# Performance work log

Measured on AMD Instinct MI355X. Metric: run time of the kernel, lower is better.

Reference implementation:

```python
import jax, jax.numpy as jnp
import numpy as np

B, S, HID, NH, HD = 2, 2048, 1024, 16, 64
SCALE = 1.0 / np.sqrt(HD)
NEG = -1e9


def _rope_cache(seq_len, dim, base=10000.0):
    inv_freq = 1.0 / (base ** (np.arange(0, dim, 2, dtype=np.float32) / dim))
    t = np.arange(seq_len, dtype=np.float32)
    freqs = np.outer(t, inv_freq)                      # [S, dim/2]
    emb = np.concatenate([freqs, freqs], axis=-1)      # [S, dim]
    return jnp.asarray(np.cos(emb)), jnp.asarray(np.sin(emb))


def _rotate_half(x):
    x1, x2 = jnp.split(x, 2, axis=-1)
    return jnp.concatenate([-x2, x1], axis=-1)


def setup_inputs() -> dict:
    key = jax.random.key(0)
    k0, k1, k2, k3, k4 = jax.random.split(key, 5)
    hidden_states = jax.random.normal(k0, (B, S, HID), jnp.float32)
    Wq = jax.random.normal(k1, (HID, NH * HD), jnp.float32) * 0.02
    Wk = jax.random.normal(k2, (HID, NH * HD), jnp.float32) * 0.02
    Wv = jax.random.normal(k3, (HID, NH * HD), jnp.float32) * 0.02
    Wo = jax.random.normal(k4, (NH * HD, HID), jnp.float32) * 0.02
    causal = jnp.tril(jnp.ones((S, S), bool))
    attention_mask = jnp.broadcast_to(
        jnp.where(causal, 0.0, NEG).astype(jnp.float32)[None, None], (B, 1, S, S))
    position_ids = jnp.broadcast_to(jnp.arange(S, dtype=jnp.int32)[None], (B, S))
    cos, sin = _rope_cache(S, HD)
    return {"hidden_states": hidden_states, "attention_mask": attention_mask,
            "position_ids": position_ids, "cos": cos, "sin": sin,
            "Wq": Wq, "Wk": Wk, "Wv": Wv, "Wo": Wo}


def reference(hidden_states, attention_mask, position_ids, cos, sin, Wq, Wk, Wv, Wo):
    b, s, _ = hidden_states.shape
    def proj(W):  # [B,S,HID] @ [HID,NH*HD] -> [B,NH,S,HD]
        return jnp.einsum('bsh,hd->bsd', hidden_states, W).reshape(b, s, NH, HD).transpose(0, 2, 1, 3)
    q, k, v = proj(Wq), proj(Wk), proj(Wv)
    # RoPE: gather per-position cos/sin -> [B,1,S,HD]
    cos_g = cos[position_ids][:, None]
    sin_g = sin[position_ids][:, None]
    q = q * cos_g + _rotate_half(q) * sin_g
    k = k * cos_g + _rotate_half(k) * sin_g
    scores = jnp.einsum('bhqd,bhkd->bhqk', q, k) * SCALE + attention_mask
    attn = jax.nn.softmax(scores.astype(jnp.float32), axis=-1).astype(q.dtype)
    out = jnp.einsum('bhqk,bhkd->bhqd', attn, v)
    out = out.transpose(0, 2, 1, 3).reshape(b, s, NH * HD)
    return jnp.einsum('bsd,dh->bsh', out, Wo)
```

## Files before the change

kernel.cpp:

```cpp
#include <hip/hip_runtime.h>

typedef __bf16 bf16x8 __attribute__((ext_vector_type(8)));
typedef float  f32x4  __attribute__((ext_vector_type(4)));
typedef unsigned short ushortx8 __attribute__((ext_vector_type(8)));
typedef unsigned short ushortx4 __attribute__((ext_vector_type(4)));

static __device__ __forceinline__ unsigned short f2bf(float f) {
  unsigned int u = __builtin_bit_cast(unsigned int, f);
  u += 0x7FFFu + ((u >> 16) & 1u);
  return (unsigned short)(u >> 16);
}
static __device__ __forceinline__ unsigned short f2bf_fast(float f) {
  unsigned int u = __builtin_bit_cast(unsigned int, f);
  return (unsigned short)((u + 0x8000u) >> 16);
}

#define GLL16(gp, lp) __builtin_amdgcn_global_load_lds(                       \
    (const __attribute__((address_space(1))) void*)(gp),                      \
    (__attribute__((address_space(3))) void*)(lp), 16, 0, 0)

__global__ __launch_bounds__(256) void prep_kernel(const float* __restrict__ X,
                                                   const float* __restrict__ W0,
                                                   const float* __restrict__ W1,
                                                   const float* __restrict__ W2,
                                                   const float* __restrict__ W3,
                                                   unsigned short* __restrict__ Xbf,
                                                   unsigned short* __restrict__ D0,
                                                   unsigned short* __restrict__ D1,
                                                   unsigned short* __restrict__ D2,
                                                   unsigned short* __restrict__ D3) {
  int z = blockIdx.z;
  if (z >= 4) {
    long bid = (long)(z - 4) * 1024 + blockIdx.y * 32 + blockIdx.x;
    int tl = threadIdx.y * 32 + threadIdx.x;
    long i = bid * 2048 + (long)tl * 8;
    float4 f0 = *(const float4*)(X + i);
    float4 f1 = *(const float4*)(X + i + 4);
    ushortx8 u;
    u[0] = f2bf(f0.x); u[1] = f2bf(f0.y); u[2] = f2bf(f0.z); u[3] = f2bf(f0.w);
    u[4] = f2bf(f1.x); u[5] = f2bf(f1.y); u[6] = f2bf(f1.z); u[7] = f2bf(f1.w);
    *(ushortx8*)(Xbf + i) = u;
    return;
  }
  const float* src = (z == 0) ? W0 : (z == 1) ? W1 : (z == 2) ? W2 : W3;
  unsigned short* dst = (z == 0) ? D0 : (z == 1) ? D1 : (z == 2) ? D2 : D3;
  const int R = 1024, C = 1024;
  __shared__ unsigned short t[32][33];
  int c = blockIdx.x * 32 + threadIdx.x;
#pragma unroll
  for (int i = 0; i < 4; ++i) {
    int r = blockIdx.y * 32 + threadIdx.y + i * 8;
    t[threadIdx.y + i * 8][threadIdx.x] = f2bf(src[(size_t)r * C + c]);
  }
  __syncthreads();
  int rr = blockIdx.y * 32 + threadIdx.x;
#pragma unroll
  for (int i = 0; i < 4; ++i) {
    int cc = blockIdx.x * 32 + threadIdx.y + i * 8;
    dst[(size_t)cc * R + rr] = t[threadIdx.x][threadIdx.y + i * 8];
  }
}

__global__ __launch_bounds__(256) void gemm128_kernel(
    const unsigned short* __restrict__ A,
    const unsigned short* __restrict__ BT0,
    const unsigned short* __restrict__ BT1,
    const unsigned short* __restrict__ BT2,
    unsigned short* __restrict__ outQ,
    unsigned short* __restrict__ outK,
    unsigned short* __restrict__ outVT,
    const int* __restrict__ pos_ids,
    const float* __restrict__ cosb,
    const float* __restrict__ sinb) {
  const int K = 1024;
  int id = blockIdx.x + 8 * (blockIdx.y + 32 * blockIdx.z);
  int m_idx = id & 31;
  int nzi = id >> 5;
  int n_idx = nzi & 7;
  int z = nzi >> 3;
  const unsigned short* BT = (z == 0) ? BT0 : (z == 1 ? BT1 : BT2);
  int n0 = n_idx * 128, m0 = m_idx * 128;
  int t = threadIdx.x, lane = t & 63, w = t >> 6;
  int wy = w >> 1, wx = w & 1;
  int n16 = lane & 15, quad = lane >> 4;
  __shared__ __align__(16) unsigned short sA0[128 * 32];
  __shared__ __align__(16) unsigned short sA1[128 * 32];
  __shared__ __align__(16) unsigned short sB0[128 * 32];
  __shared__ __align__(16) unsigned short sB1[128 * 32];

  int r4 = lane >> 2, c4 = lane & 3;
  const char* gA = (const char*)(A + (size_t)(m0 + w * 32 + r4) * K) + ((c4 ^ (r4 & 3)) * 16);
  const char* gB = (const char*)(BT + (size_t)(n0 + w * 32 + r4) * K) + ((c4 ^ (r4 & 3)) * 16);
  const size_t row16 = (size_t)16 * K * 2;

  f32x4 acc[4][4];
#pragma unroll
  for (int i = 0; i < 4; ++i)
#pragma unroll
    for (int j = 0; j < 4; ++j) acc[i][j] = f32x4{0.f, 0.f, 0.f, 0.f};

#define GSTAGE(kk_, SA, SB)                                                     \
  do {                                                                          \
    GLL16(gA + (size_t)(kk_) * 2, SA + (w * 32) * 32);                          \
    GLL16(gA + (size_t)(kk_) * 2 + row16, SA + (w * 32 + 16) * 32);             \
    GLL16(gB + (size_t)(kk_) * 2, SB + (w * 32) * 32);                          \
    GLL16(gB + (size_t)(kk_) * 2 + row16, SB + (w * 32 + 16) * 32);             \
  } while (0)

#define GCOMPUTE(SA, SB)                                                        \
  do {                                                                          \
    bf16x8 a[4], b[4];                                                          \
    int cs = (quad ^ (n16 & 3)) * 8;                                            \
    _Pragma("unroll") for (int i = 0; i < 4; ++i) {                             \
      a[i] = *(const bf16x8*)(&SA[(wy * 64 + i * 16 + n16) * 32 + cs]);         \
      b[i] = *(const bf16x8*)(&SB[(wx * 64 + i * 16 + n16) * 32 + cs]);         \
    }                                                                           \
    _Pragma("unroll") for (int mt = 0; mt < 4; ++mt)                            \
      _Pragma("unroll") for (int nt = 0; nt < 4; ++nt)                          \
        acc[mt][nt] = __builtin_amdgcn_mfma_f32_16x16x32_bf16(                  \
            a[mt], b[nt], acc[mt][nt], 0, 0, 0);                                \
  } while (0)

  GSTAGE(0, sA0, sB0);
  for (int kk = 0; kk < K;) {
    __syncthreads();
    if (kk + 32 < K) GSTAGE(kk + 32, sA1, sB1);
    GCOMPUTE(sA0, sB0);
    kk += 32;
    if (kk >= K) break;
    __syncthreads();
    if (kk + 32 < K) GSTAGE(kk + 32, sA0, sB0);
    GCOMPUTE(sA1, sB1);
    kk += 32;
  }
#undef GSTAGE
#undef GCOMPUTE

  if (z < 2) {
    const float qs = (z == 0) ? (0.125f * 1.44269504088896340736f) : 1.0f;
#pragma unroll
    for (int mt = 0; mt < 4; ++mt)
#pragma unroll
      for (int r = 0; r < 4; ++r) {
        int row = m0 + wy * 64 + mt * 16 + quad * 4 + r;
        int b = row >> 11, s = row & 2047;
        int pos = pos_ids[b * 2048 + s];
        const float* cb = cosb + (size_t)pos * 64;
        const float* sb = sinb + (size_t)pos * 64;
#pragma unroll
        for (int nt = 0; nt < 2; ++nt) {
          int d0 = nt * 16 + n16;
          float c0 = cb[d0] * qs, s0 = sb[d0] * qs;
          float c1 = cb[d0 + 32] * qs, s1 = sb[d0 + 32] * qs;
          float x0 = acc[mt][nt][r], x1 = acc[mt][nt + 2][r];
          acc[mt][nt][r]     = x0 * c0 - x1 * s0;
          acc[mt][nt + 2][r] = x1 * c1 + x0 * s1;
        }
      }
  }

  if (z == 2) {
#pragma unroll
    for (int mt = 0; mt < 4; ++mt)
#pragma unroll
      for (int nt = 0; nt < 4; ++nt) {
        int row = m0 + wy * 64 + mt * 16 + quad * 4;
        int b = row >> 11, s = row & 2047;
        int col = n0 + wx * 64 + nt * 16 + n16;
        int h = col >> 6, d = col & 63;
        ushortx4 u;
#pragma unroll
        for (int r = 0; r < 4; ++r) u[r] = f2bf(acc[mt][nt][r]);
        *(ushortx4*)(&outVT[(((size_t)b * 16 + h) * 64 + d) * 2048 + s]) = u;
      }
    return;
  }

#pragma unroll
  for (int mt = 0; mt < 4; ++mt)
#pragma unroll
    for (int nt = 0; nt < 4; ++nt)
#pragma unroll
      for (int r = 0; r < 4; ++r) {
        int row = m0 + wy * 64 + mt * 16 + quad * 4 + r;
        int col = n0 + wx * 64 + nt * 16 + n16;
        unsigned short* dst = (z == 0) ? outQ : outK;
        int b = row >> 11, s = row & 2047, h = col >> 6, d = col & 63;
        dst[(((size_t)b * 16 + h) * 2048 + s) * 64 + d] = f2bf(acc[mt][nt][r]);
      }
}

__global__ __launch_bounds__(256) void gemm64_kernel(const unsigned short* __restrict__ A,
                                                     const unsigned short* __restrict__ BT,
                                                     float* __restrict__ outF) {
  const int K = 1024, N = 1024;
  int m0 = blockIdx.x * 64, n0 = blockIdx.y * 64;
  int t = threadIdx.x, lane = t & 63, w = t >> 6;
  int wy = w >> 1, wx = w & 1;
  int n16 = lane & 15, quad = lane >> 4;
  __shared__ __align__(16) unsigned short sA0[64 * 32];
  __shared__ __align__(16) unsigned short sA1[64 * 32];
  __shared__ __align__(16) unsigned short sB0[64 * 32];
  __shared__ __align__(16) unsigned short sB1[64 * 32];

  int r4 = lane >> 2, c4 = lane & 3;
  const char* gA = (const char*)(A + (size_t)(m0 + w * 16 + r4) * K) + ((c4 ^ (r4 & 3)) * 16);
  const char* gB = (const char*)(BT + (size_t)(n0 + w * 16 + r4) * K) + ((c4 ^ (r4 & 3)) * 16);

  f32x4 acc[2][2];
#pragma unroll
  for (int i = 0; i < 2; ++i)
#pragma unroll
    for (int j = 0; j < 2; ++j) acc[i][j] = f32x4{0.f, 0.f, 0.f, 0.f};

#define WSTAGE(kk_, SA, SB)                                                     \
  do {                                                                          \
    GLL16(gA + (size_t)(kk_) * 2, SA + (w * 16) * 32);                          \
    GLL16(gB + (size_t)(kk_) * 2, SB + (w * 16) * 32);                          \
  } while (0)

#define WCOMPUTE(SA, SB)                                                        \
  do {                                                                          \
    int cs = (quad ^ (n16 & 3)) * 8;                                            \
    bf16x8 a0 = *(const bf16x8*)(&SA[(wy * 32 + n16) * 32 + cs]);               \
    bf16x8 a1 = *(const bf16x8*)(&SA[(wy * 32 + 16 + n16) * 32 + cs]);          \
    bf16x8 b0 = *(const bf16x8*)(&SB[(wx * 32 + n16) * 32 + cs]);               \
    bf16x8 b1 = *(const bf16x8*)(&SB[(wx * 32 + 16 + n16) * 32 + cs]);          \
    acc[0][0] = __builtin_amdgcn_mfma_f32_16x16x32_bf16(a0, b0, acc[0][0], 0, 0, 0); \
    acc[0][1] = __builtin_amdgcn_mfma_f32_16x16x32_bf16(a0, b1, acc[0][1], 0, 0, 0); \
    acc[1][0] = __builtin_amdgcn_mfma_f32_16x16x32_bf16(a1, b0, acc[1][0], 0, 0, 0); \
    acc[1][1] = __builtin_amdgcn_mfma_f32_16x16x32_bf16(a1, b1, acc[1][1], 0, 0, 0); \
  } while (0)

  WSTAGE(0, sA0, sB0);
  for (int kk = 0; kk < K;) {
    __syncthreads();
    if (kk + 32 < K) WSTAGE(kk + 32, sA1, sB1);
    WCOMPUTE(sA0, sB0);
    kk += 32;
    if (kk >= K) break;
    __syncthreads();
    if (kk + 32 < K) WSTAGE(kk + 32, sA0, sB0);
    WCOMPUTE(sA1, sB1);
    kk += 32;
  }
#undef WSTAGE
#undef WCOMPUTE

#pragma unroll
  for (int mt = 0; mt < 2; ++mt)
#pragma unroll
    for (int nt = 0; nt < 2; ++nt)
#pragma unroll
      for (int r = 0; r < 4; ++r) {
        int row = m0 + wy * 32 + mt * 16 + quad * 4 + r;
        int col = n0 + wx * 32 + nt * 16 + n16;
        outF[(size_t)row * N + col] = acc[mt][nt][r];
      }
}

__global__ __launch_bounds__(512) void attn_kernel(const unsigned short* __restrict__ Q,
                                                   const unsigned short* __restrict__ Kk,
                                                   const unsigned short* __restrict__ VT,
                                                   unsigned short* __restrict__ O) {
  int bh = blockIdx.x;
  int qt = (int)(gridDim.y - 1 - blockIdx.y);
  int t = threadIdx.x;
  int lane = t & 63;
  int w = t >> 6;
  int g = w >> 2;
  int w4 = w & 3;
  int n16 = lane & 15, quad = lane >> 4;
  int r8 = lane >> 3, c8 = lane & 7;
  const unsigned short* Qb = Q + (size_t)bh * 2048 * 64;
  const unsigned short* Kb = Kk + (size_t)bh * 2048 * 64;
  const unsigned short* Vb = VT + (size_t)bh * 64 * 2048;

  __shared__ __align__(16) unsigned short sKV[2 * 2 * 2 * 4096];
  __shared__ __align__(16) unsigned short sP[8][16 * 64];
  unsigned short* spW = sP[w];
  unsigned short* gBase = sKV + g * 16384;

  int b_ = bh >> 4, h_ = bh & 15;
  int nk = qt + 1;
  int u = (nk + 1) >> 1;
  int beg = g ? u : 0;
  int end = g ? nk : u;
  int qg = qt * 64 + w4 * 16 + n16;

  bf16x8 aQ[2];
#pragma unroll
  for (int kb = 0; kb < 2; ++kb)
    aQ[kb] = *(const bf16x8*)(Qb + (size_t)qg * 64 + kb * 32 + quad * 8);

  f32x4 o[4];
  float mst = -3e38f, lst = 0.f;
#pragma unroll
  for (int ct = 0; ct < 4; ++ct) o[ct] = f32x4{0.f, 0.f, 0.f, 0.f};

#define ASTAGE(kt_, BUF)                                                                  \
  do {                                                                                    \
    const unsigned short* kg_ = Kb + (size_t)((kt_) * 64 + w4 * 16) * 64;                 \
    const unsigned short* vg_ = Vb + (size_t)(w4 * 16) * 2048 + (kt_) * 64;               \
    unsigned short* dK = gBase + (BUF) * 8192 + (w4 * 16) * 64;                           \
    unsigned short* dV = dK + 4096;                                                       \
    GLL16(kg_ + (size_t)r8 * 64 + (c8 ^ r8) * 8, dK);                                     \
    GLL16(kg_ + (size_t)(8 + r8) * 64 + (c8 ^ r8) * 8, dK + 8 * 64);                      \
    GLL16(vg_ + (size_t)r8 * 2048 + (c8 ^ r8) * 8, dV);                                   \
    GLL16(vg_ + (size_t)(8 + r8) * 2048 + (c8 ^ r8) * 8, dV + 8 * 64);                    \
  } while (0)

#define ACOMPUTE(kt_, BUF)                                                                \
  do {                                                                                    \
    const unsigned short* kT_ = gBase + (BUF) * 8192;                                     \
    const unsigned short* vT_ = kT_ + 4096;                                               \
    f32x4 sc[4];                                \
    _Pragma("unroll") for (int mt = 0; mt < 4; ++mt) {                                    \
      const unsigned short* kr = &kT_[(mt * 16 + n16) * 64];                              \
      bf16x8 ka0 = *(const bf16x8*)(kr + ((quad ^ (n16 & 7)) * 8));                       \
      bf16x8 ka1 = *(const bf16x8*)(kr + (((4 + quad) ^ (n16 & 7)) * 8));                 \
      f32x4 zv = f32x4{0.f, 0.f, 0.f, 0.f};                                               \
      zv = __builtin_amdgcn_mfma_f32_16x16x32_bf16(ka0, aQ[0], zv, 0, 0, 0);              \
      sc[mt] = __builtin_amdgcn_mfma_f32_16x16x32_bf16(ka1, aQ[1], zv, 0, 0, 0);          \
    }                                                                                     \
    float p[4][4];                                                                        \
    _Pragma("unroll") for (int mt = 0; mt < 4; ++mt)                                      \
      _Pragma("unroll") for (int r = 0; r < 4; ++r) p[mt][r] = sc[mt][r];                 \
    if ((kt_) == nk - 1) {                                 \
      int kb0 = (kt_) * 64 + quad * 4;                                                    \
      _Pragma("unroll") for (int mt = 0; mt < 4; ++mt)                                    \
        _Pragma("unroll") for (int r = 0; r < 4; ++r)                                     \
          if (kb0 + mt * 16 + r > qg) p[mt][r] = -3e38f;                                  \
    }                                                                                     \
    float rm = p[0][0];                                                                   \
    _Pragma("unroll") for (int mt = 0; mt < 4; ++mt)                                      \
      _Pragma("unroll") for (int r = 0; r < 4; ++r) rm = fmaxf(rm, p[mt][r]);             \
    rm = fmaxf(rm, __shfl_xor(rm, 16));                                                   \
    rm = fmaxf(rm, __shfl_xor(rm, 32));                                                   \
    float mn = fmaxf(mst, rm);                                                            \
    float al = exp2f(mst - mn);                                                           \
    mst = mn;                                                                             \
    float rs = 0.f;                                                                       \
    _Pragma("unroll") for (int mt = 0; mt < 4; ++mt)                                      \
      _Pragma("unroll") for (int r = 0; r < 4; ++r) {                                     \
        p[mt][r] = exp2f(p[mt][r] - mn);                                                  \
        rs += p[mt][r];                                                                   \
      }                                                                                   \
    lst = lst * al + rs;                                                                  \
    _Pragma("unroll") for (int ct = 0; ct < 4; ++ct)                                      \
      _Pragma("unroll") for (int r = 0; r < 4; ++r) o[ct][r] *= al;                       \
    _Pragma("unroll") for (int mt = 0; mt < 4; ++mt) {                                    \
      ushortx4 uu;                                                                        \
      _Pragma("unroll") for (int r = 0; r < 4; ++r) uu[r] = f2bf_fast(p[mt][r]);          \
      int ch = (mt * 2 + (quad >> 1)) ^ (n16 & 7);                                        \
      *(ushortx4*)(&spW[n16 * 64 + ch * 8 + (quad & 1) * 4]) = uu;                        \
    }                                                                                     \
    __builtin_amdgcn_s_waitcnt(0xC07F);     \
    bf16x8 aP0 = *(const bf16x8*)(&spW[n16 * 64 + ((quad ^ (n16 & 7)) * 8)]);             \
    bf16x8 aP1 = *(const bf16x8*)(&spW[n16 * 64 + (((4 + quad) ^ (n16 & 7)) * 8)]);       \
    _Pragma("unroll") for (int ct = 0; ct < 4; ++ct) {                                    \
      const unsigned short* vr = &vT_[(ct * 16 + n16) * 64];                              \
      bf16x8 va0 = *(const bf16x8*)(vr + ((quad ^ (n16 & 7)) * 8));                       \
      bf16x8 va1 = *(const bf16x8*)(vr + (((4 + quad) ^ (n16 & 7)) * 8));                 \
      o[ct] = __builtin_amdgcn_mfma_f32_16x16x32_bf16(va0, aP0, o[ct], 0, 0, 0);          \
      o[ct] = __builtin_amdgcn_mfma_f32_16x16x32_bf16(va1, aP1, o[ct], 0, 0, 0);          \
    }                                                                                     \
  } while (0)

  if (beg < end) ASTAGE(beg, 0);
  int it = 0;
  while (it < u) {
    __syncthreads();
    {
      int kt = beg + it;
      if (kt + 1 < end) ASTAGE(kt + 1, 1);
      if (kt < end) ACOMPUTE(kt, 0);
    }
    if (++it >= u) break;
    __syncthreads();
    {
      int kt = beg + it;
      if (kt + 1 < end) ASTAGE(kt + 1, 0);
      if (kt < end) ACOMPUTE(kt, 1);
    }
    ++it;
  }
#undef ASTAGE
#undef ACOMPUTE

  lst += __shfl_xor(lst, 16);
  lst += __shfl_xor(lst, 32);

  __syncthreads();
  float* scratch = (float*)sKV;
  int sidx = (w4 * 64 + lane) * 18;
  if (g == 1) {
#pragma unroll
    for (int ct = 0; ct < 4; ++ct)
#pragma unroll
      for (int r = 0; r < 4; ++r) scratch[sidx + ct * 4 + r] = o[ct][r];
    scratch[sidx + 16] = mst;
    scratch[sidx + 17] = lst;
  }
  __syncthreads();
  if (g == 0) {
    float m1 = scratch[sidx + 16], l1 = scratch[sidx + 17];
    float m = fmaxf(mst, m1);
    float a0 = exp2f(mst - m), a1 = exp2f(m1 - m);
    float inv = 1.0f / (lst * a0 + l1 * a1);
#pragma unroll
    for (int ct = 0; ct < 4; ++ct) {
      ushortx4 uo;
#pragma unroll
      for (int r = 0; r < 4; ++r) {
        float v = (o[ct][r] * a0 + scratch[sidx + ct * 4 + r] * a1) * inv;
        uo[r] = f2bf(v);
      }
      size_t addr = ((size_t)b_ * 2048 + qg) * 1024 + h_ * 64 + ct * 16 + quad * 4;
      *(ushortx4*)(&O[addr]) = uo;
    }
  }
}

extern "C" void kernel_launch(void* const* d_in, const int* in_sizes, int n_in,
                              void* d_out, int out_size, void* d_ws, size_t ws_size,
                              hipStream_t stream) {
  const float* X    = (const float*)d_in[0];
  const int*   pos  = (const int*)d_in[2];
  const float* cosb = (const float*)d_in[3];
  const float* sinb = (const float*)d_in[4];
  const float* Wq   = (const float*)d_in[5];
  const float* Wk   = (const float*)d_in[6];
  const float* Wv   = (const float*)d_in[7];
  const float* Wo   = (const float*)d_in[8];
  float* out = (float*)d_out;

  char* ws = (char*)d_ws;
  const size_t SZ_X = 4096UL * 1024 * 2;
  const size_t SZ_W = 1024UL * 1024 * 2;
  unsigned short* Xbf = (unsigned short*)(ws);
  unsigned short* WTq = (unsigned short*)(ws + SZ_X);
  unsigned short* WTk = (unsigned short*)(ws + SZ_X + SZ_W);
  unsigned short* WTv = (unsigned short*)(ws + SZ_X + 2 * SZ_W);
  unsigned short* WTo = (unsigned short*)(ws + SZ_X + 3 * SZ_W);
  unsigned short* Qbf = (unsigned short*)(ws + SZ_X + 4 * SZ_W);
  unsigned short* Kbf = (unsigned short*)(ws + 2 * SZ_X + 4 * SZ_W);
  unsigned short* VTr = (unsigned short*)(ws + 3 * SZ_X + 4 * SZ_W);
  unsigned short* Obf = (unsigned short*)(ws + 4 * SZ_X + 4 * SZ_W);

  prep_kernel<<<dim3(32, 32, 6), dim3(32, 8), 0, stream>>>(
      X, Wq, Wk, Wv, Wo, Xbf, WTq, WTk, WTv, WTo);

  gemm128_kernel<<<dim3(8, 32, 3), 256, 0, stream>>>(Xbf, WTq, WTk, WTv,
                                                     Qbf, Kbf, VTr,
                                                     pos, cosb, sinb);

  attn_kernel<<<dim3(32, 32), 512, 0, stream>>>(Qbf, Kbf, VTr, Obf);

  gemm64_kernel<<<dim3(64, 16), 256, 0, stream>>>(Obf, WTo, out);
}
```

Before: 209.9 us.

## Fuse all stages into one persistent cooperative kernel with grid syncs

Replaces the four separate launches (prep, QKV GEMM, attention, output GEMM) with a single cooperative kernel of 256 persistent blocks that separates the phases with grid.sync. The GEMMs now use a 3-buffer LDS ring with explicit vmcnt waits, and each block loops over the three projections. Attention blocks process several query tiles each, and the softmax skips the rescale when the running max grows by no more than a threshold. This targets launch gaps and tail effects, but each grid barrier costs time, the grid is limited to 256 blocks (fewer than the old grids), and the lazy rescale slightly changes numerics.

Result: slower. 480.2 us (+128.7%).

```diff
diff --git a/kernel.cpp b/kernel.cpp
--- a/kernel.cpp
+++ b/kernel.cpp
@@ -1,4 +1,7 @@
 #include <hip/hip_runtime.h>
+#include <hip/hip_cooperative_groups.h>
+
+namespace cg = cooperative_groups;
 
 typedef __bf16 bf16x8 __attribute__((ext_vector_type(8)));
 typedef float  f32x4  __attribute__((ext_vector_type(4)));
@@ -19,284 +22,218 @@
     (const __attribute__((address_space(1))) void*)(gp),                      \
     (__attribute__((address_space(3))) void*)(lp), 16, 0, 0)
 
-__global__ __launch_bounds__(256) void prep_kernel(const float* __restrict__ X,
-                                                   const float* __restrict__ W0,
-                                                   const float* __restrict__ W1,
-                                                   const float* __restrict__ W2,
-                                                   const float* __restrict__ W3,
-                                                   unsigned short* __restrict__ Xbf,
-                                                   unsigned short* __restrict__ D0,
-                                                   unsigned short* __restrict__ D1,
-                                                   unsigned short* __restrict__ D2,
-                                                   unsigned short* __restrict__ D3) {
-  int z = blockIdx.z;
-  if (z >= 4) {
-    long bid = (long)(z - 4) * 1024 + blockIdx.y * 32 + blockIdx.x;
-    int tl = threadIdx.y * 32 + threadIdx.x;
-    long i = bid * 2048 + (long)tl * 8;
-    float4 f0 = *(const float4*)(X + i);
-    float4 f1 = *(const float4*)(X + i + 4);
-    ushortx8 u;
-    u[0] = f2bf(f0.x); u[1] = f2bf(f0.y); u[2] = f2bf(f0.z); u[3] = f2bf(f0.w);
-    u[4] = f2bf(f1.x); u[5] = f2bf(f1.y); u[6] = f2bf(f1.z); u[7] = f2bf(f1.w);
-    *(ushortx8*)(Xbf + i) = u;
-    return;
-  }
-  const float* src = (z == 0) ? W0 : (z == 1) ? W1 : (z == 2) ? W2 : W3;
-  unsigned short* dst = (z == 0) ? D0 : (z == 1) ? D1 : (z == 2) ? D2 : D3;
-  const int R = 1024, C = 1024;
-  __shared__ unsigned short t[32][33];
-  int c = blockIdx.x * 32 + threadIdx.x;
-#pragma unroll
-  for (int i = 0; i < 4; ++i) {
-    int r = blockIdx.y * 32 + threadIdx.y + i * 8;
-    t[threadIdx.y + i * 8][threadIdx.x] = f2bf(src[(size_t)r * C + c]);
-  }
-  __syncthreads();
-  int rr = blockIdx.y * 32 + threadIdx.x;
-#pragma unroll
-  for (int i = 0; i < 4; ++i) {
-    int cc = blockIdx.x * 32 + threadIdx.y + i * 8;
-    dst[(size_t)cc * R + rr] = t[threadIdx.x][threadIdx.y + i * 8];
-  }
-}
-
-__global__ __launch_bounds__(256) void gemm128_kernel(
-    const unsigned short* __restrict__ A,
-    const unsigned short* __restrict__ BT0,
-    const unsigned short* __restrict__ BT1,
-    const unsigned short* __restrict__ BT2,
-    unsigned short* __restrict__ outQ,
-    unsigned short* __restrict__ outK,
-    unsigned short* __restrict__ outVT,
-    const int* __restrict__ pos_ids,
-    const float* __restrict__ cosb,
-    const float* __restrict__ sinb) {
+struct FusedParams {
+  const float* X;
+  const int* pos;
+  const float* cosb;
+  const float* sinb;
+  const float* Wq;
+  const float* Wk;
+  const float* Wv;
+  const float* Wo;
+  unsigned short* Xbf;
+  unsigned short* WTq;
+  unsigned short* WTk;
+  unsigned short* WTv;
+  unsigned short* WTo;
+  unsigned short* Qbf;
+  unsigned short* Kbf;
+  unsigned short* VTr;
+  unsigned short* Obf;
+  float* out;
+};
+
+__device__ __forceinline__ void gemm_ring128(
+    const unsigned short* __restrict__ A, const unsigned short* __restrict__ BT,
+    int m0, int n0, int t, f32x4 (&acc)[2][4],
+    unsigned short* sA, unsigned short* sB, unsigned short* sDm) {
   const int K = 1024;
-  int id = blockIdx.x + 8 * (blockIdx.y + 32 * blockIdx.z);
-  int m_idx = id & 31;
-  int nzi = id >> 5;
-  int n_idx = nzi & 7;
-  int z = nzi >> 3;
-  const unsigned short* BT = (z == 0) ? BT0 : (z == 1 ? BT1 : BT2);
-  int n0 = n_idx * 128, m0 = m_idx * 128;
-  int t = threadIdx.x, lane = t & 63, w = t >> 6;
+  const int BUFE = 128 * 32;
+  int lane = t & 63, w = t >> 6;
   int wy = w >> 1, wx = w & 1;
   int n16 = lane & 15, quad = lane >> 4;
-  __shared__ __align__(16) unsigned short sA0[128 * 32];
-  __shared__ __align__(16) unsigned short sA1[128 * 32];
-  __shared__ __align__(16) unsigned short sB0[128 * 32];
-  __shared__ __align__(16) unsigned short sB1[128 * 32];
-
-  int r4 = lane >> 2, c4 = lane & 3;
-  const char* gA = (const char*)(A + (size_t)(m0 + w * 32 + r4) * K) + ((c4 ^ (r4 & 3)) * 16);
-  const char* gB = (const char*)(BT + (size_t)(n0 + w * 32 + r4) * K) + ((c4 ^ (r4 & 3)) * 16);
-  const size_t row16 = (size_t)16 * K * 2;
-
-  f32x4 acc[4][4];
-#pragma unroll
-  for (int i = 0; i < 4; ++i)
-#pragma unroll
-    for (int j = 0; j < 4; ++j) acc[i][j] = f32x4{0.f, 0.f, 0.f, 0.f};
-
-#define GSTAGE(kk_, SA, SB)                                                     \
+  int schunk = (lane & 3) ^ ((lane >> 2) & 3);
+  const unsigned short* gA0 = A + (size_t)(m0 + w * 16 + (lane >> 2)) * K + schunk * 8;
+  const unsigned short* gB0 = BT + (size_t)(n0 + w * 16 + (lane >> 2)) * K + schunk * 8;
+  unsigned short* stA = sA + (w * 16) * 32;
+  unsigned short* stB = sB + (w * 16) * 32;
+  int cs = (quad ^ (n16 & 3)) * 8;
+  const unsigned short* rdA = sA + (wy * 32 + n16) * 32 + cs;
+  const unsigned short* rdB = sB + (wx * 64 + n16) * 32 + cs;
+  bf16x8 a[2], bb[4];
+
+#define GSTG(tt, DA, DB)                                                        \
   do {                                                                          \
-    GLL16(gA + (size_t)(kk_) * 2, SA + (w * 32) * 32);                          \
-    GLL16(gA + (size_t)(kk_) * 2 + row16, SA + (w * 32 + 16) * 32);             \
-    GLL16(gB + (size_t)(kk_) * 2, SB + (w * 32) * 32);                          \
-    GLL16(gB + (size_t)(kk_) * 2 + row16, SB + (w * 32 + 16) * 32);             \
+    GLL16(gA0 + (size_t)(tt) * 32, (DA));                                       \
+    GLL16(gB0 + (size_t)(tt) * 32, (DB));                                       \
   } while (0)
-
-#define GCOMPUTE(SA, SB)                                                        \
+#define GRD(bufi)                                                               \
   do {                                                                          \
-    bf16x8 a[4], b[4];                                                          \
-    int cs = (quad ^ (n16 & 3)) * 8;                                            \
-    _Pragma("unroll") for (int i = 0; i < 4; ++i) {                             \
-      a[i] = *(const bf16x8*)(&SA[(wy * 64 + i * 16 + n16) * 32 + cs]);         \
-      b[i] = *(const bf16x8*)(&SB[(wx * 64 + i * 16 + n16) * 32 + cs]);         \
-    }                                                                           \
-    _Pragma("unroll") for (int mt = 0; mt < 4; ++mt)                            \
-      _Pragma("unroll") for (int nt = 0; nt < 4; ++nt)                          \
-        acc[mt][nt] = __builtin_amdgcn_mfma_f32_16x16x32_bf16(                  \
-            a[mt], b[nt], acc[mt][nt], 0, 0, 0);                                \
+    _Pragma("unroll") for (int i = 0; i < 2; ++i)                               \
+      a[i] = *(const bf16x8*)(rdA + (bufi) * BUFE + i * 16 * 32);               \
+    _Pragma("unroll") for (int j = 0; j < 4; ++j)                               \
+      bb[j] = *(const bf16x8*)(rdB + (bufi) * BUFE + j * 16 * 32);              \
   } while (0)
-
-  GSTAGE(0, sA0, sB0);
-  for (int kk = 0; kk < K;) {
-    __syncthreads();
-    if (kk + 32 < K) GSTAGE(kk + 32, sA1, sB1);
-    GCOMPUTE(sA0, sB0);
-    kk += 32;
-    if (kk >= K) break;
-    __syncthreads();
-    if (kk + 32 < K) GSTAGE(kk + 32, sA0, sB0);
-    GCOMPUTE(sA1, sB1);
-    kk += 32;
+#define GMM                                                                     \
+  do {                                                                          \
+    _Pragma("unroll") for (int i = 0; i < 2; ++i)                               \
+      _Pragma("unroll") for (int j = 0; j < 4; ++j)                             \
+        acc[i][j] = __builtin_amdgcn_mfma_f32_16x16x32_bf16(                    \
+            a[i], bb[j], acc[i][j], 0, 0, 0);                                   \
+  } while (0)
+
+  GSTG(0, stA, stB);
+  GSTG(1, stA + BUFE, stB + BUFE);
+  asm volatile("s_waitcnt vmcnt(2)" ::: "memory");
+  __builtin_amdgcn_s_barrier();
+
+#pragma unroll 3
+  for (int kt = 0; kt < 30; ++kt) {
+    int buf = kt % 3, pfb = (kt + 2) % 3;
+    GRD(buf);
+    GSTG(kt + 2, stA + pfb * BUFE, stB + pfb * BUFE);
+    GMM;
+    asm volatile("s_waitcnt vmcnt(2)" ::: "memory");
+    __builtin_amdgcn_s_barrier();
   }
-#undef GSTAGE
-#undef GCOMPUTE
-
-  if (z < 2) {
-    const float qs = (z == 0) ? (0.125f * 1.44269504088896340736f) : 1.0f;
-#pragma unroll
-    for (int mt = 0; mt < 4; ++mt)
-#pragma unroll
-      for (int r = 0; r < 4; ++r) {
-        int row = m0 + wy * 64 + mt * 16 + quad * 4 + r;
-        int b = row >> 11, s = row & 2047;
-        int pos = pos_ids[b * 2048 + s];
-        const float* cb = cosb + (size_t)pos * 64;
-        const float* sb = sinb + (size_t)pos * 64;
-#pragma unroll
-        for (int nt = 0; nt < 2; ++nt) {
-          int d0 = nt * 16 + n16;
-          float c0 = cb[d0] * qs, s0 = sb[d0] * qs;
-          float c1 = cb[d0 + 32] * qs, s1 = sb[d0 + 32] * qs;
-          float x0 = acc[mt][nt][r], x1 = acc[mt][nt + 2][r];
-          acc[mt][nt][r]     = x0 * c0 - x1 * s0;
-          acc[mt][nt + 2][r] = x1 * c1 + x0 * s1;
-        }
+  GRD(0);
+  GSTG(31, sDm, sDm);
+  GMM;
+  asm volatile("s_waitcnt vmcnt(2)" ::: "memory");
+  __builtin_amdgcn_s_barrier();
+  GRD(1);
+  GSTG(31, sDm, sDm);
+  GMM;
+  asm volatile("s_waitcnt vmcnt(0)" ::: "memory");
+#undef GSTG
+#undef GRD
+#undef GMM
+}
+
+__global__ __launch_bounds__(512, 2) void fused_kernel(FusedParams p) {
+  __shared__ __align__(16) unsigned char smem[81920];
+  cg::grid_group grid = cg::this_grid();
+  int b = blockIdx.x, t = threadIdx.x;
+  int lane = t & 63, w = t >> 6;
+  int n16 = lane & 15, quad = lane >> 4;
+
+  {
+    size_t base = ((size_t)b * 512 + t) * 8;
+#pragma unroll
+    for (int p4 = 0; p4 < 4; ++p4) {
+      size_t i = base + (size_t)p4 * (131072 * 8);
+      float4 f0 = *(const float4*)(p.X + i);
+      float4 f1 = *(const float4*)(p.X + i + 4);
+      ushortx8 u;
+      u[0] = f2bf(f0.x); u[1] = f2bf(f0.y); u[2] = f2bf(f0.z); u[3] = f2bf(f0.w);
+      u[4] = f2bf(f1.x); u[5] = f2bf(f1.y); u[6] = f2bf(f1.z); u[7] = f2bf(f1.w);
+      *(ushortx8*)(p.Xbf + i) = u;
+    }
+    unsigned short (*tl)[32][33] = (unsigned short (*)[32][33])smem;
+    int sub = t >> 8;
+    int t256 = t & 255;
+    int tx = t256 & 31, ty = t256 >> 5;
+    for (int it = 0; it < 8; ++it) {
+      int tid = b * 16 + it * 2 + sub;
+      int mat = tid >> 10, rem = tid & 1023;
+      int trow = rem >> 5, tcol = rem & 31;
+      const float* src = (mat == 0) ? p.Wq : (mat == 1) ? p.Wk : (mat == 2) ? p.Wv : p.Wo;
+      unsigned short* dst = (mat == 0) ? p.WTq : (mat == 1) ? p.WTk : (mat == 2) ? p.WTv : p.WTo;
+#pragma unroll
+      for (int r = 0; r < 4; ++r)
+        tl[sub][ty + r * 8][tx] = f2bf(src[(size_t)(trow * 32 + ty + r * 8) * 1024 + tcol * 32 + tx]);
+      __syncthreads();
+#pragma unroll
+      for (int r = 0; r < 4; ++r)
+        dst[(size_t)(tcol * 32 + ty + r * 8) * 1024 + trow * 32 + tx] = tl[sub][tx][ty + r * 8];
+      __syncthreads();
+    }
+  }
+  __threadfence();
+  grid.sync();
+
+  {
+    unsigned short* sA = (unsigned short*)smem;
+    unsigned short* sB = (unsigned short*)(smem + 24576);
+    unsigned short* sDm = (unsigned short*)(smem + 49152);
+    int m0 = (b & 31) * 128, n0 = ((b >> 5) & 7) * 128;
+    int wy = w >> 1, wx = w & 1;
+    for (int z = 0; z < 3; ++z) {
+      if (z) __syncthreads();
+      const unsigned short* BTz = (z == 0) ? p.WTq : (z == 1 ? p.WTk : p.WTv);
+      f32x4 acc[2][4];
+#pragma unroll
+      for (int i = 0; i < 2; ++i)
+#pragma unroll
+        for (int j = 0; j < 4; ++j) acc[i][j] = f32x4{0.f, 0.f, 0.f, 0.f};
+      gemm_ring128(p.Xbf, BTz, m0, n0, t, acc, sA, sB, sDm);
+
+      if (z < 2) {
+        const float qs = (z == 0) ? (0.125f * 1.44269504088896340736f) : 1.0f;
+#pragma unroll
+        for (int mt = 0; mt < 2; ++mt)
+#pragma unroll
+          for (int r = 0; r < 4; ++r) {
+            int row = m0 + wy * 32 + mt * 16 + quad * 4 + r;
+            int b_ = row >> 11, s_ = row & 2047;
+            int pos = p.pos[b_ * 2048 + s_];
+            const float* cb = p.cosb + (size_t)pos * 64;
+            const float* sb = p.sinb + (size_t)pos * 64;
+#pragma unroll
+            for (int nt = 0; nt < 2; ++nt) {
+              int d0 = nt * 16 + n16;
+              float c0 = cb[d0] * qs, s0 = sb[d0] * qs;
+              float c1 = cb[d0 + 32] * qs, s1 = sb[d0 + 32] * qs;
+              float x0 = acc[mt][nt][r], x1 = acc[mt][nt + 2][r];
+              acc[mt][nt][r]     = x0 * c0 - x1 * s0;
+              acc[mt][nt + 2][r] = x1 * c1 + x0 * s1;
+            }
+          }
+        unsigned short* dst = (z == 0) ? p.Qbf : p.Kbf;
+#pragma unroll
+        for (int mt = 0; mt < 2; ++mt)
+#pragma unroll
+          for (int nt = 0; nt < 4; ++nt)
+#pragma unroll
+            for (int r = 0; r < 4; ++r) {
+              int row = m0 + wy * 32 + mt * 16 + quad * 4 + r;
+              int col = n0 + wx * 64 + nt * 16 + n16;
+              int b_ = row >> 11, s_ = row & 2047, h_ = col >> 6, d_ = col & 63;
+              dst[(((size_t)b_ * 16 + h_) * 2048 + s_) * 64 + d_] = f2bf(acc[mt][nt][r]);
+            }
+      } else {
+#pragma unroll
+        for (int mt = 0; mt < 2; ++mt)
+#pragma unroll
+          for (int nt = 0; nt < 4; ++nt) {
+            int row = m0 + wy * 32 + mt * 16 + quad * 4;
+            int b_ = row >> 11, s_ = row & 2047;
+            int col = n0 + wx * 64 + nt * 16 + n16;
+            int h_ = col >> 6, d_ = col & 63;
+            ushortx4 u;
+#pragma unroll
+            for (int r = 0; r < 4; ++r) u[r] = f2bf(acc[mt][nt][r]);
+            *(ushortx4*)(&p.VTr[(((size_t)b_ * 16 + h_) * 64 + d_) * 2048 + s_]) = u;
+          }
       }
+    }
   }
-
-  if (z == 2) {
-#pragma unroll
-    for (int mt = 0; mt < 4; ++mt)
-#pragma unroll
-      for (int nt = 0; nt < 4; ++nt) {
-        int row = m0 + wy * 64 + mt * 16 + quad * 4;
-        int b = row >> 11, s = row & 2047;
-        int col = n0 + wx * 64 + nt * 16 + n16;
-        int h = col >> 6, d = col & 63;
-        ushortx4 u;
-#pragma unroll
-        for (int r = 0; r < 4; ++r) u[r] = f2bf(acc[mt][nt][r]);
-        *(ushortx4*)(&outVT[(((size_t)b * 16 + h) * 64 + d) * 2048 + s]) = u;
-      }
-    return;
-  }
-
-#pragma unroll
-  for (int mt = 0; mt < 4; ++mt)
-#pragma unroll
-    for (int nt = 0; nt < 4; ++nt)
-#pragma unroll
-      for (int r = 0; r < 4; ++r) {
-        int row = m0 + wy * 64 + mt * 16 + quad * 4 + r;
-        int col = n0 + wx * 64 + nt * 16 + n16;
-        unsigned short* dst = (z == 0) ? outQ : outK;
-        int b = row >> 11, s = row & 2047, h = col >> 6, d = col & 63;
-        dst[(((size_t)b * 16 + h) * 2048 + s) * 64 + d] = f2bf(acc[mt][nt][r]);
-      }
-}
-
-__global__ __launch_bounds__(256) void gemm64_kernel(const unsigned short* __restrict__ A,
-                                                     const unsigned short* __restrict__ BT,
-                                                     float* __restrict__ outF) {
-  const int K = 1024, N = 1024;
-  int m0 = blockIdx.x * 64, n0 = blockIdx.y * 64;
-  int t = threadIdx.x, lane = t & 63, w = t >> 6;
-  int wy = w >> 1, wx = w & 1;
-  int n16 = lane & 15, quad = lane >> 4;
-  __shared__ __align__(16) unsigned short sA0[64 * 32];
-  __shared__ __align__(16) unsigned short sA1[64 * 32];
-  __shared__ __align__(16) unsigned short sB0[64 * 32];
-  __shared__ __align__(16) unsigned short sB1[64 * 32];
-
-  int r4 = lane >> 2, c4 = lane & 3;
-  const char* gA = (const char*)(A + (size_t)(m0 + w * 16 + r4) * K) + ((c4 ^ (r4 & 3)) * 16);
-  const char* gB = (const char*)(BT + (size_t)(n0 + w * 16 + r4) * K) + ((c4 ^ (r4 & 3)) * 16);
-
-  f32x4 acc[2][2];
-#pragma unroll
-  for (int i = 0; i < 2; ++i)
-#pragma unroll
-    for (int j = 0; j < 2; ++j) acc[i][j] = f32x4{0.f, 0.f, 0.f, 0.f};
-
-#define WSTAGE(kk_, SA, SB)                                                     \
-  do {                                                                          \
-    GLL16(gA + (size_t)(kk_) * 2, SA + (w * 16) * 32);                          \
-    GLL16(gB + (size_t)(kk_) * 2, SB + (w * 16) * 32);                          \
-  } while (0)
-
-#define WCOMPUTE(SA, SB)                                                        \
-  do {                                                                          \
-    int cs = (quad ^ (n16 & 3)) * 8;                                            \
-    bf16x8 a0 = *(const bf16x8*)(&SA[(wy * 32 + n16) * 32 + cs]);               \
-    bf16x8 a1 = *(const bf16x8*)(&SA[(wy * 32 + 16 + n16) * 32 + cs]);          \
-    bf16x8 b0 = *(const bf16x8*)(&SB[(wx * 32 + n16) * 32 + cs]);               \
-    bf16x8 b1 = *(const bf16x8*)(&SB[(wx * 32 + 16 + n16) * 32 + cs]);          \
-    acc[0][0] = __builtin_amdgcn_mfma_f32_16x16x32_bf16(a0, b0, acc[0][0], 0, 0, 0); \
-    acc[0][1] = __builtin_amdgcn_mfma_f32_16x16x32_bf16(a0, b1, acc[0][1], 0, 0, 0); \
-    acc[1][0] = __builtin_amdgcn_mfma_f32_16x16x32_bf16(a1, b0, acc[1][0], 0, 0, 0); \
-    acc[1][1] = __builtin_amdgcn_mfma_f32_16x16x32_bf16(a1, b1, acc[1][1], 0, 0, 0); \
-  } while (0)
-
-  WSTAGE(0, sA0, sB0);
-  for (int kk = 0; kk < K;) {
-    __syncthreads();
-    if (kk + 32 < K) WSTAGE(kk + 32, sA1, sB1);
-    WCOMPUTE(sA0, sB0);
-    kk += 32;
-    if (kk >= K) break;
-    __syncthreads();
-    if (kk + 32 < K) WSTAGE(kk + 32, sA0, sB0);
-    WCOMPUTE(sA1, sB1);
-    kk += 32;
-  }
-#undef WSTAGE
-#undef WCOMPUTE
-
-#pragma unroll
-  for (int mt = 0; mt < 2; ++mt)
-#pragma unroll
-    for (int nt = 0; nt < 2; ++nt)
-#pragma unroll
-      for (int r = 0; r < 4; ++r) {
-        int row = m0 + wy * 32 + mt * 16 + quad * 4 + r;
-        int col = n0 + wx * 32 + nt * 16 + n16;
-        outF[(size_t)row * N + col] = acc[mt][nt][r];
-      }
-}
-
-__global__ __launch_bounds__(512) void attn_kernel(const unsigned short* __restrict__ Q,
-                                                   const unsigned short* __restrict__ Kk,
-                                                   const unsigned short* __restrict__ VT,
-                                                   unsigned short* __restrict__ O) {
-  int bh = blockIdx.x;
-  int qt = (int)(gridDim.y - 1 - blockIdx.y);
-  int t = threadIdx.x;
-  int lane = t & 63;
-  int w = t >> 6;
-  int g = w >> 2;
-  int w4 = w & 3;
-  int n16 = lane & 15, quad = lane >> 4;
-  int r8 = lane >> 3, c8 = lane & 7;
-  const unsigned short* Qb = Q + (size_t)bh * 2048 * 64;
-  const unsigned short* Kb = Kk + (size_t)bh * 2048 * 64;
-  const unsigned short* Vb = VT + (size_t)bh * 64 * 2048;
-
-  __shared__ __align__(16) unsigned short sKV[2 * 2 * 2 * 4096];
-  __shared__ __align__(16) unsigned short sP[8][16 * 64];
-  unsigned short* spW = sP[w];
-  unsigned short* gBase = sKV + g * 16384;
-
-  int b_ = bh >> 4, h_ = bh & 15;
-  int nk = qt + 1;
-  int u = (nk + 1) >> 1;
-  int beg = g ? u : 0;
-  int end = g ? nk : u;
-  int qg = qt * 64 + w4 * 16 + n16;
-
-  bf16x8 aQ[2];
-#pragma unroll
-  for (int kb = 0; kb < 2; ++kb)
-    aQ[kb] = *(const bf16x8*)(Qb + (size_t)qg * 64 + kb * 32 + quad * 8);
-
-  f32x4 o[4];
-  float mst = -3e38f, lst = 0.f;
-#pragma unroll
-  for (int ct = 0; ct < 4; ++ct) o[ct] = f32x4{0.f, 0.f, 0.f, 0.f};
+  __threadfence();
+  grid.sync();
+
+  {
+    unsigned short* sKV = (unsigned short*)smem;
+    unsigned short* sP = (unsigned short*)(smem + 65536);
+    int g = w >> 2, w4 = w & 3;
+    int r8 = lane >> 3, c8 = lane & 7;
+    unsigned short* spW = sP + w * 1024;
+    unsigned short* gBase = sKV + g * 16384;
+    int slot = b & 7, bh = b >> 3;
+    int b_ = bh >> 4, h_ = bh & 15;
+    const unsigned short* Qb = p.Qbf + (size_t)bh * 2048 * 64;
+    const unsigned short* Kb = p.Kbf + (size_t)bh * 2048 * 64;
+    const unsigned short* Vb = p.VTr + (size_t)bh * 64 * 2048;
+    int qts[4] = {31 - slot, 16 + slot, 15 - slot, slot};
 
 #define ASTAGE(kt_, BUF)                                                                  \
   do {                                                                                    \
@@ -323,35 +260,38 @@
       zv = __builtin_amdgcn_mfma_f32_16x16x32_bf16(ka0, aQ[0], zv, 0, 0, 0);              \
       sc[mt] = __builtin_amdgcn_mfma_f32_16x16x32_bf16(ka1, aQ[1], zv, 0, 0, 0);          \
     }                                                                                     \
-    float p[4][4];                                                                        \
+    float pp[4][4];                                                                       \
     _Pragma("unroll") for (int mt = 0; mt < 4; ++mt)                                      \
-      _Pragma("unroll") for (int r = 0; r < 4; ++r) p[mt][r] = sc[mt][r];                 \
+      _Pragma("unroll") for (int r = 0; r < 4; ++r) pp[mt][r] = sc[mt][r];                \
     if ((kt_) == nk - 1) {                                 \
       int kb0 = (kt_) * 64 + quad * 4;                                                    \
       _Pragma("unroll") for (int mt = 0; mt < 4; ++mt)                                    \
         _Pragma("unroll") for (int r = 0; r < 4; ++r)                                     \
-          if (kb0 + mt * 16 + r > qg) p[mt][r] = -3e38f;                                  \
+          if (kb0 + mt * 16 + r > qg) pp[mt][r] = -3e38f;                                 \
     }                                                                                     \
-    float rm = p[0][0];                                                                   \
+    float rm = pp[0][0];                                                                  \
     _Pragma("unroll") for (int mt = 0; mt < 4; ++mt)                                      \
-      _Pragma("unroll") for (int r = 0; r < 4; ++r) rm = fmaxf(rm, p[mt][r]);             \
+      _Pragma("unroll") for (int r = 0; r < 4; ++r) rm = fmaxf(rm, pp[mt][r]);            \
     rm = fmaxf(rm, __shfl_xor(rm, 16));                                                   \
     rm = fmaxf(rm, __shfl_xor(rm, 32));                                                   \
-    float mn = fmaxf(mst, rm);                                                            \
-    float al = exp2f(mst - mn);                                                           \
-    mst = mn;                                                                             \
+    if (!__all(rm <= mst + 8.f)) {                                     \
+      float mn = fmaxf(mst, rm);                                                          \
+      float al = exp2f(mst - mn);                                                         \
+      mst = mn;                                                                           \
+      lst *= al;                                                                          \
+      _Pragma("unroll") for (int ct = 0; ct < 4; ++ct)                                    \
+        _Pragma("unroll") for (int r = 0; r < 4; ++r) o[ct][r] *= al;                     \
+    }                                                                                     \
     float rs = 0.f;                                                                       \
     _Pragma("unroll") for (int mt = 0; mt < 4; ++mt)                                      \
       _Pragma("unroll") for (int r = 0; r < 4; ++r) {                                     \
-        p[mt][r] = exp2f(p[mt][r] - mn);                                                  \
-        rs += p[mt][r];                                                                   \
+        pp[mt][r] = exp2f(pp[mt][r] - mst);                                               \
+        rs += pp[mt][r];                                                                  \
       }                                                                                   \
-    lst = lst * al + rs;                                                                  \
-    _Pragma("unroll") for (int ct = 0; ct < 4; ++ct)                                      \
-      _Pragma("unroll") for (int r = 0; r < 4; ++r) o[ct][r] *= al;                       \
+    lst += rs;                                                                            \
     _Pragma("unroll") for (int mt = 0; mt < 4; ++mt) {                                    \
       ushortx4 uu;                                                                        \
-      _Pragma("unroll") for (int r = 0; r < 4; ++r) uu[r] = f2bf_fast(p[mt][r]);          \
+      _Pragma("unroll") for (int r = 0; r < 4; ++r) uu[r] = f2bf_fast(pp[mt][r]);         \
       int ch = (mt * 2 + (quad >> 1)) ^ (n16 & 7);                                        \
       *(ushortx4*)(&spW[n16 * 64 + ch * 8 + (quad & 1) * 4]) = uu;                        \
     }                                                                                     \
@@ -367,58 +307,105 @@
     }                                                                                     \
   } while (0)
 
-  if (beg < end) ASTAGE(beg, 0);
-  int it = 0;
-  while (it < u) {
-    __syncthreads();
-    {
-      int kt = beg + it;
-      if (kt + 1 < end) ASTAGE(kt + 1, 1);
-      if (kt < end) ACOMPUTE(kt, 0);
+    for (int ui = 0; ui < 4; ++ui) {
+      __syncthreads();
+      int qt = qts[ui];
+      int nk = qt + 1;
+      int u = (nk + 1) >> 1;
+      int beg = g ? u : 0;
+      int end = g ? nk : u;
+      int qg = qt * 64 + w4 * 16 + n16;
+
+      bf16x8 aQ[2];
+#pragma unroll
+      for (int kb = 0; kb < 2; ++kb)
+        aQ[kb] = *(const bf16x8*)(Qb + (size_t)qg * 64 + kb * 32 + quad * 8);
+
+      f32x4 o[4];
+      float mst = -3e38f, lst = 0.f;
+#pragma unroll
+      for (int ct = 0; ct < 4; ++ct) o[ct] = f32x4{0.f, 0.f, 0.f, 0.f};
+
+      if (beg < end) ASTAGE(beg, 0);
+      int it = 0;
+      while (it < u) {
+        __syncthreads();
+        {
+          int kt = beg + it;
+          if (kt + 1 < end) ASTAGE(kt + 1, 1);
+          if (kt < end) ACOMPUTE(kt, 0);
+        }
+        if (++it >= u) break;
+        __syncthreads();
+        {
+          int kt = beg + it;
+          if (kt + 1 < end) ASTAGE(kt + 1, 0);
+          if (kt < end) ACOMPUTE(kt, 1);
+        }
+        ++it;
+      }
+
+      lst += __shfl_xor(lst, 16);
+      lst += __shfl_xor(lst, 32);
+
+      __syncthreads();
+      float* scratch = (float*)sKV;
+      int sidx = (w4 * 64 + lane) * 18;
+      if (g == 1) {
+#pragma unroll
+        for (int ct = 0; ct < 4; ++ct)
+#pragma unroll
+          for (int r = 0; r < 4; ++r) scratch[sidx + ct * 4 + r] = o[ct][r];
+        scratch[sidx + 16] = mst;
+        scratch[sidx + 17] = lst;
+      }
+      __syncthreads();
+      if (g == 0) {
+        float m1 = scratch[sidx + 16], l1 = scratch[sidx + 17];
+        float m = fmaxf(mst, m1);
+        float a0 = exp2f(mst - m), a1 = exp2f(m1 - m);
+        float inv = 1.0f / (lst * a0 + l1 * a1);
+#pragma unroll
+        for (int ct = 0; ct < 4; ++ct) {
+          ushortx4 uo;
+#pragma unroll
+          for (int r = 0; r < 4; ++r) {
+            float v = (o[ct][r] * a0 + scratch[sidx + ct * 4 + r] * a1) * inv;
+            uo[r] = f2bf(v);
+          }
+          size_t addr = ((size_t)b_ * 2048 + qg) * 1024 + h_ * 64 + ct * 16 + quad * 4;
+          *(ushortx4*)(&p.Obf[addr]) = uo;
+        }
+      }
     }
-    if (++it >= u) break;
-    __syncthreads();
-    {
-      int kt = beg + it;
-      if (kt + 1 < end) ASTAGE(kt + 1, 0);
-      if (kt < end) ACOMPUTE(kt, 1);
-    }
-    ++it;
-  }
 #undef ASTAGE
 #undef ACOMPUTE
-
-  lst += __shfl_xor(lst, 16);
-  lst += __shfl_xor(lst, 32);
-
-  __syncthreads();
-  float* scratch = (float*)sKV;
-  int sidx = (w4 * 64 + lane) * 18;
-  if (g == 1) {
-#pragma unroll
-    for (int ct = 0; ct < 4; ++ct)
-#pragma unroll
-      for (int r = 0; r < 4; ++r) scratch[sidx + ct * 4 + r] = o[ct][r];
-    scratch[sidx + 16] = mst;
-    scratch[sidx + 17] = lst;
   }
-  __syncthreads();
-  if (g == 0) {
-    float m1 = scratch[sidx + 16], l1 = scratch[sidx + 17];
-    float m = fmaxf(mst, m1);
-    float a0 = exp2f(mst - m), a1 = exp2f(m1 - m);
-    float inv = 1.0f / (lst * a0 + l1 * a1);
-#pragma unroll
-    for (int ct = 0; ct < 4; ++ct) {
-      ushortx4 uo;
-#pragma unroll
-      for (int r = 0; r < 4; ++r) {
-        float v = (o[ct][r] * a0 + scratch[sidx + ct * 4 + r] * a1) * inv;
-        uo[r] = f2bf(v);
-      }
-      size_t addr = ((size_t)b_ * 2048 + qg) * 1024 + h_ * 64 + ct * 16 + quad * 4;
-      *(ushortx4*)(&O[addr]) = uo;
-    }
+  __threadfence();
+  grid.sync();
+
+  {
+    unsigned short* sA = (unsigned short*)smem;
+    unsigned short* sB = (unsigned short*)(smem + 24576);
+    unsigned short* sDm = (unsigned short*)(smem + 49152);
+    int m0 = (b & 31) * 128, n0 = (b >> 5) * 128;
+    int wy = w >> 1, wx = w & 1;
+    f32x4 acc[2][4];
+#pragma unroll
+    for (int i = 0; i < 2; ++i)
+#pragma unroll
+      for (int j = 0; j < 4; ++j) acc[i][j] = f32x4{0.f, 0.f, 0.f, 0.f};
+    gemm_ring128(p.Obf, p.WTo, m0, n0, t, acc, sA, sB, sDm);
+#pragma unroll
+    for (int mt = 0; mt < 2; ++mt)
+#pragma unroll
+      for (int nt = 0; nt < 4; ++nt)
+#pragma unroll
+        for (int r = 0; r < 4; ++r) {
+          int row = m0 + wy * 32 + mt * 16 + quad * 4 + r;
+          int col = n0 + wx * 64 + nt * 16 + n16;
+          p.out[(size_t)row * 1024 + col] = acc[mt][nt][r];
+        }
   }
 }
 
@@ -448,14 +435,8 @@
   unsigned short* VTr = (unsigned short*)(ws + 3 * SZ_X + 4 * SZ_W);
   unsigned short* Obf = (unsigned short*)(ws + 4 * SZ_X + 4 * SZ_W);
 
-  prep_kernel<<<dim3(32, 32, 6), dim3(32, 8), 0, stream>>>(
-      X, Wq, Wk, Wv, Wo, Xbf, WTq, WTk, WTv, WTo);
-
-  gemm128_kernel<<<dim3(8, 32, 3), 256, 0, stream>>>(Xbf, WTq, WTk, WTv,
-                                                     Qbf, Kbf, VTr,
-                                                     pos, cosb, sinb);
-
-  attn_kernel<<<dim3(32, 32), 512, 0, stream>>>(Qbf, Kbf, VTr, Obf);
-
-  gemm64_kernel<<<dim3(64, 16), 256, 0, stream>>>(Obf, WTo, out);
+  FusedParams params{X, pos, cosb, sinb, Wq, Wk, Wv, Wo,
+                     Xbf, WTq, WTk, WTv, WTo, Qbf, Kbf, VTr, Obf, out};
+  void* kargs[] = {&params};
+  hipLaunchCooperativeKernel((void*)fused_kernel, dim3(256), dim3(512), kargs, 0, stream);
 }
```
